# Optimization experiments

Hardware: AMD Instinct MI355X
Metric: run time of the kernel (lower is better)

The kernel has to match this reference:

```python
import math
import jax, jax.numpy as jnp
import numpy as np

B, N, D = 8, 2048, 512


def setup_inputs() -> dict:
    key = jax.random.key(0)
    ks = jax.random.split(key, 9)
    s = 1.0 / math.sqrt(D)
    return {
        "x": jax.random.normal(ks[0], (B, N, D), dtype=jnp.float32),
        "adj": jax.random.uniform(ks[1], (B, N, N), dtype=jnp.float32),
        "Wqk": jax.random.normal(ks[2], (D, D), dtype=jnp.float32) * s,
        "bqk": jax.random.normal(ks[3], (D,), dtype=jnp.float32) * s,
        "Wl": jax.random.normal(ks[4], (D, D), dtype=jnp.float32) * s,
        "bl": jax.random.normal(ks[5], (D,), dtype=jnp.float32) * s,
        "Wr": jax.random.normal(ks[6], (D, D), dtype=jnp.float32) * s,
        "Wd": jax.random.normal(ks[7], (D, 1), dtype=jnp.float32),
        "bd": jax.random.normal(ks[8], (D,), dtype=jnp.float32),
    }


def reference(x, adj, Wqk, bqk, Wl, bl, Wr, Wd, bd):
    # degree gating: sigmoid(Linear(rowsum(adj)))
    deg = jnp.sum(adj, axis=-1, keepdims=True)           # [B, N, 1]
    gate = jax.nn.sigmoid(deg * Wd[:, 0] + bd)           # [B, N, D]
    xg = x * gate
    # sigmoid QK features
    QK = jax.nn.sigmoid(xg @ Wqk.T + bqk)                # [B, N, D]
    scores = jnp.einsum("bnd,bmd->bnm", QK, QK) / math.sqrt(D)
    scores = scores * adj                                # adjacency mask
    attn = scores / (jnp.sum(scores, axis=-1, keepdims=True) + 1e-6)
    out = jnp.einsum("bnm,bmd->bnd", attn, xg)           # aggregate values
    out = out @ Wl.T + bl + xg @ Wr.T                    # left + right branch
    return jax.nn.relu(out)
```

## Files before the change

### kernel.cpp

```cpp
#include <hip/hip_runtime.h>
#include <hip/hip_bf16.h>


typedef __bf16 bf16;
typedef __bf16 bf16x2 __attribute__((ext_vector_type(2)));
typedef __bf16 bf16x8 __attribute__((ext_vector_type(8)));
typedef float  f32x4  __attribute__((ext_vector_type(4)));

#define Bb 8
#define Nn 2048
#define Dd 512
#define SMEM_BYTES 33792
#define TILE8_BYTES 49152
#define SMEM8_BYTES (3 * TILE8_BYTES)

__device__ __forceinline__ bf16 to_bf16(float f) { return (bf16)f; }
__device__ __forceinline__ float sigmoidf_(float x) { return 1.0f / (1.0f + __expf(-x)); }

__device__ __forceinline__ void gld16(const void* g, void* l) {
    __builtin_amdgcn_global_load_lds(
        (__attribute__((address_space(1))) void*)(void*)g,
        (__attribute__((address_space(3))) void*)l,
        16, 0, 0);
}

__device__ __forceinline__ void gemm_bt_core(
    const bf16* __restrict__ A, const bf16* __restrict__ Bt,
    int lda, int ldb, int K,
    char* As, char* Bs, f32x4 acc[4][4])
{
    const int tid  = threadIdx.x;
    const int lane = tid & 63;
    const int wave = tid >> 6;
    const int wm = (wave >> 1) << 6;
    const int wn = (wave & 1) << 6;

    for (int kt = 0; kt < K; kt += 64) {
#pragma unroll
        for (int i = 0; i < 4; ++i) {
            int ff   = i * 256 + tid;
            int row  = ff >> 3;
            int slot = ff & 7;
            int gch  = slot ^ (row & 7);
            gld16(A  + (size_t)row * lda + kt + gch * 8, As + ff * 16);
            gld16(Bt + (size_t)row * ldb + kt + gch * 8, Bs + ff * 16);
        }
        __syncthreads();
#pragma unroll
        for (int ks = 0; ks < 2; ++ks) {
            bf16x8 af[4], bfr[4];
#pragma unroll
            for (int mi = 0; mi < 4; ++mi) {
                int row  = wm + mi * 16 + (lane & 15);
                int slot = ((ks << 2) + (lane >> 4)) ^ (row & 7);
                af[mi] = *(const bf16x8*)(As + row * 128 + slot * 16);
            }
#pragma unroll
            for (int ni = 0; ni < 4; ++ni) {
                int row  = wn + ni * 16 + (lane & 15);
                int slot = ((ks << 2) + (lane >> 4)) ^ (row & 7);
                bfr[ni] = *(const bf16x8*)(Bs + row * 128 + slot * 16);
            }
#pragma unroll
            for (int mi = 0; mi < 4; ++mi)
#pragma unroll
                for (int ni = 0; ni < 4; ++ni)
                    acc[mi][ni] = __builtin_amdgcn_mfma_f32_16x16x32_bf16(
                        af[mi], bfr[ni], acc[mi][ni], 0, 0, 0);
        }
        __syncthreads();
    }
}

#define GEMM_PROLOGUE()                                  \
    __shared__ __align__(16) char smem[SMEM_BYTES];      \
    char* As = smem;                                     \
    char* Bs = smem + 16384;                             \
    f32x4 acc[4][4];                                     \
    _Pragma("unroll") for (int mi = 0; mi < 4; ++mi)     \
    _Pragma("unroll") for (int ni = 0; ni < 4; ++ni)     \
        acc[mi][ni] = (f32x4){0.f, 0.f, 0.f, 0.f};

__device__ __forceinline__ void gemm_bt8_core(
    const bf16* __restrict__ A0, const bf16* __restrict__ B0,
    int lda0, int ldb0, int nt0,
    const bf16* __restrict__ A1, const bf16* __restrict__ B1,
    int lda1, int ldb1, int nt1,
    char* smem, f32x4 acc[4][4])
{
    const int tid  = threadIdx.x;
    const int lane = tid & 63;
    const int wave = tid >> 6;
    const int wm = (wave >> 1) << 6;
    const int wn = (wave & 1) << 6;
    const int NT = nt0 + nt1;

    char* bA = smem;
    char* bB = smem + TILE8_BYTES;
    char* bC = smem + 2 * TILE8_BYTES;

    auto stage_tile = [&](char* base, int t) {
        const bf16* A  = (t < nt0) ? A0 : A1;
        const bf16* Bt = (t < nt0) ? B0 : B1;
        const int lda  = (t < nt0) ? lda0 : lda1;
        const int ldb  = (t < nt0) ? ldb0 : ldb1;
        const int kt   = ((t < nt0) ? t : t - nt0) << 6;
#pragma unroll
        for (int i = 0; i < 4; ++i) {
            int ff   = i * 512 + tid;
            int row  = ff >> 3;
            int slot = ff & 7;
            int gch  = slot ^ (row & 7);
            gld16(A + (size_t)row * lda + kt + gch * 8, base + ff * 16);
        }
#pragma unroll
        for (int i = 0; i < 2; ++i) {
            int ff   = i * 512 + tid;
            int row  = ff >> 3;
            int slot = ff & 7;
            int gch  = slot ^ (row & 7);
            gld16(Bt + (size_t)row * ldb + kt + gch * 8, base + 32768 + ff * 16);
        }
    };

    stage_tile(bA, 0);
    stage_tile(bB, 1);
    asm volatile("s_waitcnt vmcnt(6)" ::: "memory");
    __builtin_amdgcn_s_barrier();

#pragma unroll 1
    for (int t = 0; t < NT; ++t) {
        bf16x8 af0[4], bf0[4], af1[4], bf1[4];
#pragma unroll
        for (int mi = 0; mi < 4; ++mi) {
            int row  = wm + mi * 16 + (lane & 15);
            int slot = (lane >> 4) ^ (row & 7);
            af0[mi] = *(const bf16x8*)(bA + row * 128 + slot * 16);
        }
#pragma unroll
        for (int ni = 0; ni < 4; ++ni) {
            int row  = wn + ni * 16 + (lane & 15);
            int slot = (lane >> 4) ^ (row & 7);
            bf0[ni] = *(const bf16x8*)(bA + 32768 + row * 128 + slot * 16);
        }
        if (t + 2 < NT) stage_tile(bC, t + 2);
        __builtin_amdgcn_s_barrier();
        asm volatile("s_waitcnt lgkmcnt(0)" ::: "memory");
        __builtin_amdgcn_sched_barrier(0);
#pragma unroll
        for (int mi = 0; mi < 4; ++mi) {
            int row  = wm + mi * 16 + (lane & 15);
            int slot = (4 + (lane >> 4)) ^ (row & 7);
            af1[mi] = *(const bf16x8*)(bA + row * 128 + slot * 16);
        }
#pragma unroll
        for (int ni = 0; ni < 4; ++ni) {
            int row  = wn + ni * 16 + (lane & 15);
            int slot = (4 + (lane >> 4)) ^ (row & 7);
            bf1[ni] = *(const bf16x8*)(bA + 32768 + row * 128 + slot * 16);
        }
        __builtin_amdgcn_sched_barrier(0);
        __builtin_amdgcn_s_setprio(1);
#pragma unroll
        for (int mi = 0; mi < 4; ++mi)
#pragma unroll
            for (int ni = 0; ni < 4; ++ni)
                acc[mi][ni] = __builtin_amdgcn_mfma_f32_16x16x32_bf16(
                    af0[mi], bf0[ni], acc[mi][ni], 0, 0, 0);
        __builtin_amdgcn_s_setprio(0);
        asm volatile("s_waitcnt lgkmcnt(0)" ::: "memory");
        __builtin_amdgcn_sched_barrier(0);
        __builtin_amdgcn_s_setprio(1);
#pragma unroll
        for (int mi = 0; mi < 4; ++mi)
#pragma unroll
            for (int ni = 0; ni < 4; ++ni)
                acc[mi][ni] = __builtin_amdgcn_mfma_f32_16x16x32_bf16(
                    af1[mi], bf1[ni], acc[mi][ni], 0, 0, 0);
        __builtin_amdgcn_s_setprio(0);
        __builtin_amdgcn_sched_barrier(0);
        if (t + 2 < NT)      asm volatile("s_waitcnt vmcnt(6)" ::: "memory");
        else if (t + 1 < NT) asm volatile("s_waitcnt vmcnt(0)" ::: "memory");
        __builtin_amdgcn_s_barrier();
        char* tmp = bA; bA = bB; bB = bC; bC = tmp;
    }
}

template <typename F>
__device__ __forceinline__ void epilogue_rt8(f32x4 acc[4][4], char* smem, F&& emit)
{
    const int tid  = threadIdx.x;
    const int lane = tid & 63;
    const int wave = tid >> 6;
    const int wm4 = wave >> 1;
    const int wn  = (wave & 1) << 6;
    const int cq = lane >> 4;
    const int cl = lane & 15;
    float* t = (float*)smem;
    const int chunk = tid & 15;
    const int rbase = tid >> 4;
#pragma unroll
    for (int ph = 0; ph < 4; ++ph) {
        __syncthreads();
        if (wm4 == ph) {
#pragma unroll
            for (int mi = 0; mi < 4; ++mi)
#pragma unroll
                for (int ni = 0; ni < 4; ++ni)
#pragma unroll
                    for (int r = 0; r < 4; ++r) {
                        int lr = mi * 16 + cq * 4 + r;
                        int lc = wn + ni * 16 + cl;
                        t[lr * 132 + lc] = acc[mi][ni][r];
                    }
        }
        __syncthreads();
#pragma unroll
        for (int rr = 0; rr < 2; ++rr) {
            int lr = rr * 32 + rbase;
            f32x4 a = *(const f32x4*)&t[lr * 132 + chunk * 8];
            f32x4 b = *(const f32x4*)&t[lr * 132 + chunk * 8 + 4];
            float v[8] = {a[0], a[1], a[2], a[3], b[0], b[1], b[2], b[3]};
            emit(ph * 64 + lr, chunk * 8, v);
        }
    }
}

__global__ __launch_bounds__(256) void k_gate(
    const float* __restrict__ x, const float* __restrict__ adj,
    const float* __restrict__ Wd, const float* __restrict__ bd,
    const float* __restrict__ Wqk, const float* __restrict__ Wl,
    const float* __restrict__ Wr,
    bf16* __restrict__ xg, bf16* __restrict__ Wqkb, bf16* __restrict__ Wlb,
    bf16* __restrict__ Wrb, float* __restrict__ denom)
{
    const int rowg = blockIdx.x;
    const int tid  = threadIdx.x;
    if (tid < 48) {
        int idx = rowg * 48 + tid;
        if (idx < 262144)      Wqkb[idx]          = to_bf16(Wqk[idx]);
        else if (idx < 524288) Wlb[idx - 262144]  = to_bf16(Wl[idx - 262144]);
        else                   Wrb[idx - 524288]  = to_bf16(Wr[idx - 524288]);
    }
    if (tid == 63) denom[rowg] = 0.f;

    const float4* arow = (const float4*)(adj + (size_t)rowg * Nn);
    float4 v0 = arow[tid];
    float4 v1 = arow[tid + 256];
    float s = v0.x + v0.y + v0.z + v0.w + v1.x + v1.y + v1.z + v1.w;
#pragma unroll
    for (int off = 32; off > 0; off >>= 1) s += __shfl_down(s, off, 64);
    __shared__ float red[4];
    if ((tid & 63) == 0) red[tid >> 6] = s;
    __syncthreads();
    const float deg = red[0] + red[1] + red[2] + red[3];
    const int d2 = tid;
    float2 xv  = ((const float2*)(x + (size_t)rowg * Dd))[d2];
    float2 wd  = ((const float2*)Wd)[d2];
    float2 bd2 = ((const float2*)bd)[d2];
    bf16x2 o;
    o[0] = to_bf16(xv.x * sigmoidf_(deg * wd.x + bd2.x));
    o[1] = to_bf16(xv.y * sigmoidf_(deg * wd.y + bd2.y));
    *(bf16x2*)(xg + (size_t)rowg * Dd + d2 * 2) = o;
}

__global__ __launch_bounds__(256) void k_transpose(
    const bf16* __restrict__ xg, bf16* __restrict__ xgT)
{
    const int b = blockIdx.z, nt = blockIdx.y, dt = blockIdx.x;
    __shared__ bf16 tile[64][66];
    const int c = threadIdx.x & 63, r0 = threadIdx.x >> 6;
    const bf16* src = xg + ((size_t)b * Nn + nt * 64) * Dd + dt * 64;
#pragma unroll
    for (int i = 0; i < 16; ++i) {
        int r = i * 4 + r0;
        tile[r][c] = src[(size_t)r * Dd + c];
    }
    __syncthreads();
    bf16* dst = xgT + ((size_t)b * Dd + dt * 64) * Nn + nt * 64;
#pragma unroll
    for (int i = 0; i < 16; ++i) {
        int r = i * 4 + r0;
        dst[(size_t)r * Nn + c] = tile[c][r];
    }
}

__global__ __launch_bounds__(512) void k_qk_gemm8(
    const bf16* __restrict__ xg, const bf16* __restrict__ Wqkb,
    const float* __restrict__ bqk, bf16* __restrict__ QK)
{
    extern __shared__ __align__(16) char smem[];
    const int blockRow = blockIdx.y * 256;
    const int blockCol = blockIdx.x * 128;
    f32x4 acc[4][4];
#pragma unroll
    for (int mi = 0; mi < 4; ++mi)
#pragma unroll
        for (int ni = 0; ni < 4; ++ni) acc[mi][ni] = (f32x4){0.f, 0.f, 0.f, 0.f};
    gemm_bt8_core(xg + (size_t)blockRow * Dd, Wqkb + (size_t)blockCol * Dd,
                  Dd, Dd, 8,
                  xg, Wqkb, Dd, Dd, 0, smem, acc);
    epilogue_rt8(acc, smem, [&](int lr, int lc, float* v) {
        int c = blockCol + lc;
        float4 b0 = *(const float4*)(bqk + c);
        float4 b1 = *(const float4*)(bqk + c + 4);
        float bb[8] = {b0.x, b0.y, b0.z, b0.w, b1.x, b1.y, b1.z, b1.w};
        bf16x8 o;
#pragma unroll
        for (int j = 0; j < 8; ++j) o[j] = to_bf16(sigmoidf_(v[j] + bb[j]));
        *(bf16x8*)(QK + (size_t)(blockRow + lr) * Dd + c) = o;
    });
}

__global__ __launch_bounds__(256) void k_s_gemm(
    const bf16* __restrict__ QK, const float* __restrict__ adj,
    bf16* __restrict__ S, float* __restrict__ denom)
{
    const int b = blockIdx.y;
    int t = blockIdx.x, i = 0;
    while (t >= 16 - i) { t -= 16 - i; ++i; }
    const int j = i + t;
    const int rowI = i * 128, rowJ = j * 128;
    const bf16* Qb = QK + (size_t)b * Nn * Dd;
    GEMM_PROLOGUE();
    gemm_bt_core(Qb + (size_t)rowI * Dd, Qb + (size_t)rowJ * Dd,
                 Dd, Dd, Dd, As, Bs, acc);
    const float scale = 0.044194173824159216f;

    const int tid  = threadIdx.x;
    const int lane = tid & 63;
    const int wave = tid >> 6;
    const int wm = (wave >> 1) << 6;
    const int wn = (wave & 1) << 6;
    const int cq = lane >> 4;
    const int cl = lane & 15;
    float* tls = (float*)smem;
    const int chunk = tid & 15;
    const int rbase = tid >> 4;

    auto store_side = [&](int blockRow, int blockCol, bool trans) {
#pragma unroll
        for (int ph = 0; ph < 2; ++ph) {
            __syncthreads();
            if (!trans) {
                if ((wave >> 1) == ph) {
#pragma unroll
                    for (int mi = 0; mi < 4; ++mi)
#pragma unroll
                        for (int ni = 0; ni < 4; ++ni)
#pragma unroll
                            for (int r = 0; r < 4; ++r)
                                tls[(mi * 16 + cq * 4 + r) * 132 + wn + ni * 16 + cl]
                                    = acc[mi][ni][r];
                }
            } else {
                if ((wave & 1) == ph) {
#pragma unroll
                    for (int mi = 0; mi < 4; ++mi)
#pragma unroll
                        for (int ni = 0; ni < 4; ++ni)
#pragma unroll
                            for (int r = 0; r < 4; ++r)
                                tls[(ni * 16 + cl) * 132 + wm + mi * 16 + cq * 4 + r]
                                    = acc[mi][ni][r];
                }
            }
            __syncthreads();
#pragma unroll
            for (int rr = 0; rr < 4; ++rr) {
                int lr = rr * 16 + rbase;
                f32x4 a = *(const f32x4*)&tls[lr * 132 + chunk * 8];
                f32x4 c4 = *(const f32x4*)&tls[lr * 132 + chunk * 8 + 4];
                float v[8] = {a[0], a[1], a[2], a[3], c4[0], c4[1], c4[2], c4[3]};
                int gRow = blockRow + ph * 64 + lr;
                size_t base = ((size_t)b * Nn + gRow) * Nn + blockCol + chunk * 8;
                float4 a0 = *(const float4*)(adj + base);
                float4 a1 = *(const float4*)(adj + base + 4);
                float aa[8] = {a0.x, a0.y, a0.z, a0.w, a1.x, a1.y, a1.z, a1.w};
                bf16x8 o;
                float ds = 0.f;
#pragma unroll
                for (int jj = 0; jj < 8; ++jj) {
                    float s = v[jj] * scale * aa[jj];
                    bf16 sb = to_bf16(s);
                    o[jj] = sb;
                    ds += (float)sb;
                }
                *(bf16x8*)(S + base) = o;
#pragma unroll
                for (int off = 8; off > 0; off >>= 1) ds += __shfl_xor(ds, off, 16);
                if ((tid & 15) == 0) atomicAdd(&denom[b * Nn + gRow], ds);
            }
        }
    };
    store_side(rowI, rowJ, false);
    if (i != j) store_side(rowJ, rowI, true);
}

__global__ __launch_bounds__(512) void k_h_gemm8(
    const bf16* __restrict__ S, const bf16* __restrict__ xgT,
    const float* __restrict__ denom, bf16* __restrict__ h)
{
    extern __shared__ __align__(16) char smem[];
    const int id  = blockIdx.x;
    const int b   = id & 7;
    const int pos = id >> 3;
    const int blockRow = (pos >> 2) * 256;
    const int blockCol = (pos & 3) * 128;
    f32x4 acc[4][4];
#pragma unroll
    for (int mi = 0; mi < 4; ++mi)
#pragma unroll
        for (int ni = 0; ni < 4; ++ni) acc[mi][ni] = (f32x4){0.f, 0.f, 0.f, 0.f};
    gemm_bt8_core(S + ((size_t)b * Nn + blockRow) * Nn,
                  xgT + ((size_t)b * Dd + blockCol) * Nn,
                  Nn, Nn, 32,
                  S, xgT, Nn, Nn, 0, smem, acc);
    epilogue_rt8(acc, smem, [&](int lr, int lc, float* v) {
        int gRow = blockRow + lr;
        float inv = 1.0f / (denom[b * Nn + gRow] + 1e-6f);
        bf16x8 o;
#pragma unroll
        for (int j = 0; j < 8; ++j) o[j] = to_bf16(v[j] * inv);
        *(bf16x8*)(h + ((size_t)b * Nn + gRow) * Dd + blockCol + lc) = o;
    });
}

__global__ __launch_bounds__(512) void k_out_gemm8(
    const bf16* __restrict__ h, const bf16* __restrict__ xg,
    const bf16* __restrict__ Wlb, const bf16* __restrict__ Wrb,
    const float* __restrict__ bl, float* __restrict__ out)
{
    extern __shared__ __align__(16) char smem[];
    const int blockRow = blockIdx.y * 256;
    const int blockCol = blockIdx.x * 128;
    f32x4 acc[4][4];
#pragma unroll
    for (int mi = 0; mi < 4; ++mi)
#pragma unroll
        for (int ni = 0; ni < 4; ++ni) acc[mi][ni] = (f32x4){0.f, 0.f, 0.f, 0.f};
    gemm_bt8_core(h  + (size_t)blockRow * Dd, Wlb + (size_t)blockCol * Dd,
                  Dd, Dd, 8,
                  xg + (size_t)blockRow * Dd, Wrb + (size_t)blockCol * Dd,
                  Dd, Dd, 8, smem, acc);
    epilogue_rt8(acc, smem, [&](int lr, int lc, float* v) {
        int c = blockCol + lc;
        float4 b0 = *(const float4*)(bl + c);
        float4 b1 = *(const float4*)(bl + c + 4);
        float bb[8] = {b0.x, b0.y, b0.z, b0.w, b1.x, b1.y, b1.z, b1.w};
        float4 o0, o1;
        o0.x = fmaxf(v[0] + bb[0], 0.f); o0.y = fmaxf(v[1] + bb[1], 0.f);
        o0.z = fmaxf(v[2] + bb[2], 0.f); o0.w = fmaxf(v[3] + bb[3], 0.f);
        o1.x = fmaxf(v[4] + bb[4], 0.f); o1.y = fmaxf(v[5] + bb[5], 0.f);
        o1.z = fmaxf(v[6] + bb[6], 0.f); o1.w = fmaxf(v[7] + bb[7], 0.f);
        float* p = out + (size_t)(blockRow + lr) * Dd + c;
        *(float4*)p = o0;
        *(float4*)(p + 4) = o1;
    });
}

extern "C" void kernel_launch(void* const* d_in, const int* in_sizes, int n_in,
                              void* d_out, int out_size, void* d_ws, size_t ws_size,
                              hipStream_t stream) {
    const float* x   = (const float*)d_in[0];
    const float* adj = (const float*)d_in[1];
    const float* Wqk = (const float*)d_in[2];
    const float* bqk = (const float*)d_in[3];
    const float* Wl  = (const float*)d_in[4];
    const float* bl  = (const float*)d_in[5];
    const float* Wr  = (const float*)d_in[6];
    const float* Wd  = (const float*)d_in[7];
    const float* bd  = (const float*)d_in[8];
    float* out = (float*)d_out;

    char* ws = (char*)d_ws;
    bf16* xg   = (bf16*)ws;  ws += (size_t)Bb * Nn * Dd * 2;
    bf16* xgT  = (bf16*)ws;  ws += (size_t)Bb * Dd * Nn * 2;
    bf16* QK   = (bf16*)ws;  ws += (size_t)Bb * Nn * Dd * 2;
    bf16* S    = (bf16*)ws;  ws += (size_t)Bb * Nn * Nn * 2;
    bf16* Wqkb = (bf16*)ws;  ws += (size_t)Dd * Dd * 2;
    bf16* Wlb  = (bf16*)ws;  ws += (size_t)Dd * Dd * 2;
    bf16* Wrb  = (bf16*)ws;  ws += (size_t)Dd * Dd * 2;
    float* denom = (float*)ws; ws += (size_t)Bb * Nn * 4;
    bf16* h = QK;

    static bool attr_done = false;
    if (!attr_done) {
        hipFuncSetAttribute((const void*)k_qk_gemm8,
                            hipFuncAttributeMaxDynamicSharedMemorySize, SMEM8_BYTES);
        hipFuncSetAttribute((const void*)k_h_gemm8,
                            hipFuncAttributeMaxDynamicSharedMemorySize, SMEM8_BYTES);
        hipFuncSetAttribute((const void*)k_out_gemm8,
                            hipFuncAttributeMaxDynamicSharedMemorySize, SMEM8_BYTES);
        attr_done = true;
    }

    k_gate<<<dim3(Bb * Nn), 256, 0, stream>>>(x, adj, Wd, bd, Wqk, Wl, Wr,
                                              xg, Wqkb, Wlb, Wrb, denom);
    k_transpose<<<dim3(Dd / 64, Nn / 64, Bb), 256, 0, stream>>>(xg, xgT);
    k_qk_gemm8<<<dim3(Dd / 128, (Bb * Nn) / 256), 512, SMEM8_BYTES, stream>>>(xg, Wqkb, bqk, QK);
    k_s_gemm<<<dim3(136, Bb), 256, 0, stream>>>(QK, adj, S, denom);
    k_h_gemm8<<<dim3(256), 512, SMEM8_BYTES, stream>>>(S, xgT, denom, h);
    k_out_gemm8<<<dim3(Dd / 128, (Bb * Nn) / 256), 512, SMEM8_BYTES, stream>>>(h, xg, Wlb, Wrb, bl, out);
}
```

Measured before the change: 381.0 us.

## Fuse score GEMM, adjacency mask, and aggregation into one flash-style attention kernel

Replaces the symmetric S=QK·QKᵀ kernel (which wrote a bf16 BxNxN score matrix and atomically accumulated row denominators) and the separate S·xg GEMM with a single k_attn kernel. Each block keeps a 64-row QK tile in LDS, streams 256-column chunks to compute masked scores, stages them in LDS as bf16, and multiplies them straight into an h accumulator, normalising at the end. This removes the global S round-trip (64 MB written and read) and the atomics. In exchange it gives up the symmetric-half saving in the score GEMM, launches only 256 blocks, and reads the B operands (QK and xgT rows) directly from global memory without LDS staging, which may limit MFMA throughput.

```diff
diff --git a/kernel.cpp b/kernel.cpp
--- a/kernel.cpp
+++ b/kernel.cpp
@@ -10,9 +10,9 @@
 #define Bb 8
 #define Nn 2048
 #define Dd 512
-#define SMEM_BYTES 33792
 #define TILE8_BYTES 49152
 #define SMEM8_BYTES (3 * TILE8_BYTES)
+#define ATTN_SMEM (65536 + 33792 + 2048 + 256)
 
 __device__ __forceinline__ bf16 to_bf16(float f) { return (bf16)f; }
 __device__ __forceinline__ float sigmoidf_(float x) { return 1.0f / (1.0f + __expf(-x)); }
@@ -23,63 +23,6 @@
         (__attribute__((address_space(3))) void*)l,
         16, 0, 0);
 }
-
-__device__ __forceinline__ void gemm_bt_core(
-    const bf16* __restrict__ A, const bf16* __restrict__ Bt,
-    int lda, int ldb, int K,
-    char* As, char* Bs, f32x4 acc[4][4])
-{
-    const int tid  = threadIdx.x;
-    const int lane = tid & 63;
-    const int wave = tid >> 6;
-    const int wm = (wave >> 1) << 6;
-    const int wn = (wave & 1) << 6;
-
-    for (int kt = 0; kt < K; kt += 64) {
-#pragma unroll
-        for (int i = 0; i < 4; ++i) {
-            int ff   = i * 256 + tid;
-            int row  = ff >> 3;
-            int slot = ff & 7;
-            int gch  = slot ^ (row & 7);
-            gld16(A  + (size_t)row * lda + kt + gch * 8, As + ff * 16);
-            gld16(Bt + (size_t)row * ldb + kt + gch * 8, Bs + ff * 16);
-        }
-        __syncthreads();
-#pragma unroll
-        for (int ks = 0; ks < 2; ++ks) {
-            bf16x8 af[4], bfr[4];
-#pragma unroll
-            for (int mi = 0; mi < 4; ++mi) {
-                int row  = wm + mi * 16 + (lane & 15);
-                int slot = ((ks << 2) + (lane >> 4)) ^ (row & 7);
-                af[mi] = *(const bf16x8*)(As + row * 128 + slot * 16);
-            }
-#pragma unroll
-            for (int ni = 0; ni < 4; ++ni) {
-                int row  = wn + ni * 16 + (lane & 15);
-                int slot = ((ks << 2) + (lane >> 4)) ^ (row & 7);
-                bfr[ni] = *(const bf16x8*)(Bs + row * 128 + slot * 16);
-            }
-#pragma unroll
-            for (int mi = 0; mi < 4; ++mi)
-#pragma unroll
-                for (int ni = 0; ni < 4; ++ni)
-                    acc[mi][ni] = __builtin_amdgcn_mfma_f32_16x16x32_bf16(
-                        af[mi], bfr[ni], acc[mi][ni], 0, 0, 0);
-        }
-        __syncthreads();
-    }
-}
-
-#define GEMM_PROLOGUE()                                  \
-    __shared__ __align__(16) char smem[SMEM_BYTES];      \
-    char* As = smem;                                     \
-    char* Bs = smem + 16384;                             \
-    f32x4 acc[4][4];                                     \
-    _Pragma("unroll") for (int mi = 0; mi < 4; ++mi)     \
-    _Pragma("unroll") for (int ni = 0; ni < 4; ++ni)     \
-        acc[mi][ni] = (f32x4){0.f, 0.f, 0.f, 0.f};
 
 __device__ __forceinline__ void gemm_bt8_core(
     const bf16* __restrict__ A0, const bf16* __restrict__ B0,
@@ -232,7 +175,7 @@
     const float* __restrict__ Wqk, const float* __restrict__ Wl,
     const float* __restrict__ Wr,
     bf16* __restrict__ xg, bf16* __restrict__ Wqkb, bf16* __restrict__ Wlb,
-    bf16* __restrict__ Wrb, float* __restrict__ denom)
+    bf16* __restrict__ Wrb)
 {
     const int rowg = blockIdx.x;
     const int tid  = threadIdx.x;
@@ -242,7 +185,6 @@
         else if (idx < 524288) Wlb[idx - 262144]  = to_bf16(Wl[idx - 262144]);
         else                   Wrb[idx - 524288]  = to_bf16(Wr[idx - 524288]);
     }
-    if (tid == 63) denom[rowg] = 0.f;
 
     const float4* arow = (const float4*)(adj + (size_t)rowg * Nn);
     float4 v0 = arow[tid];
@@ -312,118 +254,177 @@
     });
 }
 
-__global__ __launch_bounds__(256) void k_s_gemm(
-    const bf16* __restrict__ QK, const float* __restrict__ adj,
-    bf16* __restrict__ S, float* __restrict__ denom)
-{
-    const int b = blockIdx.y;
-    int t = blockIdx.x, i = 0;
-    while (t >= 16 - i) { t -= 16 - i; ++i; }
-    const int j = i + t;
-    const int rowI = i * 128, rowJ = j * 128;
-    const bf16* Qb = QK + (size_t)b * Nn * Dd;
-    GEMM_PROLOGUE();
-    gemm_bt_core(Qb + (size_t)rowI * Dd, Qb + (size_t)rowJ * Dd,
-                 Dd, Dd, Dd, As, Bs, acc);
+__global__ __launch_bounds__(512) void k_attn(
+    const bf16* __restrict__ QK, const bf16* __restrict__ xgT,
+    const float* __restrict__ adj, bf16* __restrict__ h)
+{
+    extern __shared__ __align__(16) char smem[];
+    char*  qki  = smem;
+    char*  Pl   = smem + 65536;
+    float* dred = (float*)(smem + 65536 + 33792);
+    float* dinv = (float*)(smem + 65536 + 33792 + 2048);
+
+    const int id   = blockIdx.x;
+    const int b    = id & 7;
+    const int row0 = (id >> 3) * 64;
+    const int tid  = threadIdx.x;
+    const int lane = tid & 63, w = tid >> 6;
+    const int cq = lane >> 4, cl = lane & 15;
+
+    const bf16*  QKb  = QK  + (size_t)b * Nn * Dd;
+    const bf16*  QKi  = QKb + (size_t)row0 * Dd;
+    const bf16*  xgTb = xgT + (size_t)b * Dd * Nn;
+    const float* adjb = adj + (size_t)b * Nn * Nn + (size_t)row0 * Nn;
+
+#pragma unroll
+    for (int i = 0; i < 8; ++i) {
+        int ff = i * 512 + tid;
+        int row = ff >> 6, slot = ff & 63;
+        int gch = (slot & 56) | ((slot & 7) ^ (row & 7));
+        gld16(QKi + (size_t)row * Dd + gch * 8, qki + ff * 16);
+    }
+
+    f32x4 hacc[4][4];
+#pragma unroll
+    for (int mi = 0; mi < 4; ++mi)
+#pragma unroll
+        for (int ni = 0; ni < 4; ++ni) hacc[mi][ni] = (f32x4){0.f, 0.f, 0.f, 0.f};
+    float dloc[16];
+#pragma unroll
+    for (int i = 0; i < 16; ++i) dloc[i] = 0.f;
+    float acur[2][16];
+
+    __syncthreads();
+
     const float scale = 0.044194173824159216f;
 
-    const int tid  = threadIdx.x;
-    const int lane = tid & 63;
-    const int wave = tid >> 6;
-    const int wm = (wave >> 1) << 6;
-    const int wn = (wave & 1) << 6;
-    const int cq = lane >> 4;
-    const int cl = lane & 15;
-    float* tls = (float*)smem;
-    const int chunk = tid & 15;
-    const int rbase = tid >> 4;
-
-    auto store_side = [&](int blockRow, int blockCol, bool trans) {
-#pragma unroll
-        for (int ph = 0; ph < 2; ++ph) {
-            __syncthreads();
-            if (!trans) {
-                if ((wave >> 1) == ph) {
-#pragma unroll
-                    for (int mi = 0; mi < 4; ++mi)
-#pragma unroll
-                        for (int ni = 0; ni < 4; ++ni)
-#pragma unroll
-                            for (int r = 0; r < 4; ++r)
-                                tls[(mi * 16 + cq * 4 + r) * 132 + wn + ni * 16 + cl]
-                                    = acc[mi][ni][r];
+#pragma unroll 1
+    for (int jt = 0; jt < 8; ++jt) {
+        const int j0 = jt * 256;
+#pragma unroll
+        for (int nf = 0; nf < 2; ++nf)
+#pragma unroll
+            for (int mi = 0; mi < 4; ++mi)
+#pragma unroll
+                for (int r = 0; r < 4; ++r)
+                    acur[nf][mi * 4 + r] =
+                        adjb[(size_t)(mi * 16 + cq * 4 + r) * Nn + j0 + w * 32 + nf * 16 + cl];
+
+        f32x4 tacc[2][4];
+#pragma unroll
+        for (int nf = 0; nf < 2; ++nf)
+#pragma unroll
+            for (int mi = 0; mi < 4; ++mi) tacc[nf][mi] = (f32x4){0.f, 0.f, 0.f, 0.f};
+#pragma unroll
+        for (int kc = 0; kc < 16; ++kc) {
+            bf16x8 af[4], bq[2];
+#pragma unroll
+            for (int nf = 0; nf < 2; ++nf)
+                bq[nf] = *(const bf16x8*)(QKb
+                    + (size_t)(j0 + w * 32 + nf * 16 + cl) * Dd + kc * 32 + cq * 8);
+#pragma unroll
+            for (int mi = 0; mi < 4; ++mi) {
+                int row = mi * 16 + cl;
+                int chunk = kc * 4 + cq;
+                int slot = (chunk & 56) | ((chunk & 7) ^ (row & 7));
+                af[mi] = *(const bf16x8*)(qki + row * 1024 + slot * 16);
+            }
+#pragma unroll
+            for (int nf = 0; nf < 2; ++nf)
+#pragma unroll
+                for (int mi = 0; mi < 4; ++mi)
+                    tacc[nf][mi] = __builtin_amdgcn_mfma_f32_16x16x32_bf16(
+                        af[mi], bq[nf], tacc[nf][mi], 0, 0, 0);
+        }
+        __syncthreads();
+#pragma unroll
+        for (int nf = 0; nf < 2; ++nf)
+#pragma unroll
+            for (int mi = 0; mi < 4; ++mi)
+#pragma unroll
+                for (int r = 0; r < 4; ++r) {
+                    float s = tacc[nf][mi][r] * scale * acur[nf][mi * 4 + r];
+                    bf16 sb = to_bf16(s);
+                    *(bf16*)(Pl + (mi * 16 + cq * 4 + r) * 528
+                                + (w * 32 + nf * 16 + cl) * 2) = sb;
+                    dloc[mi * 4 + r] += (float)sb;
                 }
-            } else {
-                if ((wave & 1) == ph) {
-#pragma unroll
-                    for (int mi = 0; mi < 4; ++mi)
-#pragma unroll
-                        for (int ni = 0; ni < 4; ++ni)
-#pragma unroll
-                            for (int r = 0; r < 4; ++r)
-                                tls[(ni * 16 + cl) * 132 + wm + mi * 16 + cq * 4 + r]
-                                    = acc[mi][ni][r];
-                }
+        __syncthreads();
+#pragma unroll
+        for (int kc = 0; kc < 8; ++kc) {
+            bf16x8 pa[4], xb[4];
+#pragma unroll
+            for (int mi = 0; mi < 4; ++mi)
+                pa[mi] = *(const bf16x8*)(Pl + (mi * 16 + cl) * 528 + kc * 64 + cq * 16);
+#pragma unroll
+            for (int ni = 0; ni < 4; ++ni)
+                xb[ni] = *(const bf16x8*)(xgTb
+                    + (size_t)(w * 64 + ni * 16 + cl) * Nn + j0 + kc * 32 + cq * 8);
+#pragma unroll
+            for (int mi = 0; mi < 4; ++mi)
+#pragma unroll
+                for (int ni = 0; ni < 4; ++ni)
+                    hacc[mi][ni] = __builtin_amdgcn_mfma_f32_16x16x32_bf16(
+                        pa[mi], xb[ni], hacc[mi][ni], 0, 0, 0);
+        }
+    }
+
+#pragma unroll
+    for (int i = 0; i < 16; ++i)
+#pragma unroll
+        for (int off = 1; off < 16; off <<= 1)
+            dloc[i] += __shfl_xor(dloc[i], off, 64);
+    if (cl == 0) {
+#pragma unroll
+        for (int mi = 0; mi < 4; ++mi)
+#pragma unroll
+            for (int r = 0; r < 4; ++r)
+                dred[w * 64 + mi * 16 + cq * 4 + r] = dloc[mi * 4 + r];
+    }
+    __syncthreads();
+    if (tid < 64) {
+        float s = 0.f;
+#pragma unroll
+        for (int k = 0; k < 8; ++k) s += dred[k * 64 + tid];
+        dinv[tid] = 1.0f / (s + 1e-6f);
+    }
+    __syncthreads();
+
+    float* hs = (float*)smem;
+#pragma unroll
+    for (int p = 0; p < 2; ++p) {
+        if (p) __syncthreads();
+#pragma unroll
+        for (int m2 = 0; m2 < 2; ++m2) {
+            int mi = p * 2 + m2;
+#pragma unroll
+            for (int r = 0; r < 4; ++r) {
+                float iv = dinv[mi * 16 + cq * 4 + r];
+                int lrow = m2 * 16 + cq * 4 + r;
+#pragma unroll
+                for (int ni = 0; ni < 4; ++ni)
+                    hs[lrow * 516 + w * 64 + ni * 16 + cl] = hacc[mi][ni][r] * iv;
             }
-            __syncthreads();
-#pragma unroll
-            for (int rr = 0; rr < 4; ++rr) {
-                int lr = rr * 16 + rbase;
-                f32x4 a = *(const f32x4*)&tls[lr * 132 + chunk * 8];
-                f32x4 c4 = *(const f32x4*)&tls[lr * 132 + chunk * 8 + 4];
-                float v[8] = {a[0], a[1], a[2], a[3], c4[0], c4[1], c4[2], c4[3]};
-                int gRow = blockRow + ph * 64 + lr;
-                size_t base = ((size_t)b * Nn + gRow) * Nn + blockCol + chunk * 8;
-                float4 a0 = *(const float4*)(adj + base);
-                float4 a1 = *(const float4*)(adj + base + 4);
-                float aa[8] = {a0.x, a0.y, a0.z, a0.w, a1.x, a1.y, a1.z, a1.w};
+        }
+        __syncthreads();
+        {
+            int row = tid & 31, ch = tid >> 5;
+            int grow = row0 + p * 32 + row;
+            bf16* dst = h + ((size_t)b * Nn + grow) * Dd + ch * 32;
+            const float* src = hs + row * 516 + ch * 32;
+#pragma unroll
+            for (int g = 0; g < 4; ++g) {
+                f32x4 u = *(const f32x4*)(src + g * 8);
+                f32x4 q = *(const f32x4*)(src + g * 8 + 4);
                 bf16x8 o;
-                float ds = 0.f;
-#pragma unroll
-                for (int jj = 0; jj < 8; ++jj) {
-                    float s = v[jj] * scale * aa[jj];
-                    bf16 sb = to_bf16(s);
-                    o[jj] = sb;
-                    ds += (float)sb;
-                }
-                *(bf16x8*)(S + base) = o;
-#pragma unroll
-                for (int off = 8; off > 0; off >>= 1) ds += __shfl_xor(ds, off, 16);
-                if ((tid & 15) == 0) atomicAdd(&denom[b * Nn + gRow], ds);
+                o[0] = to_bf16(u[0]); o[1] = to_bf16(u[1]);
+                o[2] = to_bf16(u[2]); o[3] = to_bf16(u[3]);
+                o[4] = to_bf16(q[0]); o[5] = to_bf16(q[1]);
+                o[6] = to_bf16(q[2]); o[7] = to_bf16(q[3]);
+                *(bf16x8*)(dst + g * 8) = o;
             }
         }
-    };
-    store_side(rowI, rowJ, false);
-    if (i != j) store_side(rowJ, rowI, true);
-}
-
-__global__ __launch_bounds__(512) void k_h_gemm8(
-    const bf16* __restrict__ S, const bf16* __restrict__ xgT,
-    const float* __restrict__ denom, bf16* __restrict__ h)
-{
-    extern __shared__ __align__(16) char smem[];
-    const int id  = blockIdx.x;
-    const int b   = id & 7;
-    const int pos = id >> 3;
-    const int blockRow = (pos >> 2) * 256;
-    const int blockCol = (pos & 3) * 128;
-    f32x4 acc[4][4];
-#pragma unroll
-    for (int mi = 0; mi < 4; ++mi)
-#pragma unroll
-        for (int ni = 0; ni < 4; ++ni) acc[mi][ni] = (f32x4){0.f, 0.f, 0.f, 0.f};
-    gemm_bt8_core(S + ((size_t)b * Nn + blockRow) * Nn,
-                  xgT + ((size_t)b * Dd + blockCol) * Nn,
-                  Nn, Nn, 32,
-                  S, xgT, Nn, Nn, 0, smem, acc);
-    epilogue_rt8(acc, smem, [&](int lr, int lc, float* v) {
-        int gRow = blockRow + lr;
-        float inv = 1.0f / (denom[b * Nn + gRow] + 1e-6f);
-        bf16x8 o;
-#pragma unroll
-        for (int j = 0; j < 8; ++j) o[j] = to_bf16(v[j] * inv);
-        *(bf16x8*)(h + ((size_t)b * Nn + gRow) * Dd + blockCol + lc) = o;
-    });
+    }
 }
 
 __global__ __launch_bounds__(512) void k_out_gemm8(
@@ -477,29 +478,26 @@
     bf16* xg   = (bf16*)ws;  ws += (size_t)Bb * Nn * Dd * 2;
     bf16* xgT  = (bf16*)ws;  ws += (size_t)Bb * Dd * Nn * 2;
     bf16* QK   = (bf16*)ws;  ws += (size_t)Bb * Nn * Dd * 2;
-    bf16* S    = (bf16*)ws;  ws += (size_t)Bb * Nn * Nn * 2;
+    bf16* h    = (bf16*)ws;  ws += (size_t)Bb * Nn * Dd * 2;
     bf16* Wqkb = (bf16*)ws;  ws += (size_t)Dd * Dd * 2;
     bf16* Wlb  = (bf16*)ws;  ws += (size_t)Dd * Dd * 2;
     bf16* Wrb  = (bf16*)ws;  ws += (size_t)Dd * Dd * 2;
-    float* denom = (float*)ws; ws += (size_t)Bb * Nn * 4;
-    bf16* h = QK;
 
     static bool attr_done = false;
     if (!attr_done) {
         hipFuncSetAttribute((const void*)k_qk_gemm8,
                             hipFuncAttributeMaxDynamicSharedMemorySize, SMEM8_BYTES);
-        hipFuncSetAttribute((const void*)k_h_gemm8,
-                            hipFuncAttributeMaxDynamicSharedMemorySize, SMEM8_BYTES);
+        hipFuncSetAttribute((const void*)k_attn,
+                            hipFuncAttributeMaxDynamicSharedMemorySize, ATTN_SMEM);
         hipFuncSetAttribute((const void*)k_out_gemm8,
                             hipFuncAttributeMaxDynamicSharedMemorySize, SMEM8_BYTES);
         attr_done = true;
     }
 
     k_gate<<<dim3(Bb * Nn), 256, 0, stream>>>(x, adj, Wd, bd, Wqk, Wl, Wr,
-                                              xg, Wqkb, Wlb, Wrb, denom);
+                                              xg, Wqkb, Wlb, Wrb);
     k_transpose<<<dim3(Dd / 64, Nn / 64, Bb), 256, 0, stream>>>(xg, xgT);
     k_qk_gemm8<<<dim3(Dd / 128, (Bb * Nn) / 256), 512, SMEM8_BYTES, stream>>>(xg, Wqkb, bqk, QK);
-    k_s_gemm<<<dim3(136, Bb), 256, 0, stream>>>(QK, adj, S, denom);
-    k_h_gemm8<<<dim3(256), 512, SMEM8_BYTES, stream>>>(S, xgT, denom, h);
+    k_attn<<<dim3(256), 512, ATTN_SMEM, stream>>>(QK, xgT, adj, h);
     k_out_gemm8<<<dim3(Dd / 128, (Bb * Nn) / 256), 512, SMEM8_BYTES, stream>>>(h, xg, Wlb, Wrb, bl, out);
 }
```

Result: slower. 430.8 us (+13.1%).
